# Kernel tuning notes

Measured on AMD Instinct MI355X. Metric: run time of the kernel, lower is better.

Reference implementation:

```python
import jax, jax.numpy as jnp
import numpy as np

B, L, D_MODEL, D_FF, N_EXPERTS, TOP_K = 32, 256, 512, 2048, 8, 2
EPS = 1e-9


def setup_inputs() -> dict:
    key = jax.random.key(0)
    ks = jax.random.split(key, 7)
    scale1 = 1.0 / np.sqrt(D_MODEL)
    scale2 = 1.0 / np.sqrt(D_FF)
    return {
        "cycle_curve_data": jax.random.normal(ks[0], (B, L, D_MODEL), jnp.float32),
        "logits": jax.random.normal(ks[1], (B, N_EXPERTS), jnp.float32),
        "moe_masks": jax.random.randint(ks[2], (B, N_EXPERTS), 0, 2, jnp.int32),
        "W1": jax.random.normal(ks[3], (N_EXPERTS, D_MODEL, D_FF), jnp.float32) * scale1,
        "b1": jax.random.normal(ks[4], (N_EXPERTS, D_FF), jnp.float32) * scale1,
        "W2": jax.random.normal(ks[5], (N_EXPERTS, D_FF, D_MODEL), jnp.float32) * scale2,
        "b2": jax.random.normal(ks[6], (N_EXPERTS, D_MODEL), jnp.float32) * scale2,
    }


def _gates(logits, moe_masks):
    # softmax over experts, zero out unavailable experts, keep top-k, renormalize
    mask = (moe_masks == 1).astype(logits.dtype)               # [B, E]
    p = jax.nn.softmax(logits, axis=1) * mask                  # [B, E]
    _, idx = jax.lax.top_k(p, TOP_K)                           # [B, K]
    topk_mask = jnp.zeros_like(p).at[jnp.arange(p.shape[0])[:, None], idx].set(1.0)
    p = p * topk_mask
    return p / (jnp.sum(p, axis=1, keepdims=True) + EPS)       # [B, E]


def reference(cycle_curve_data, logits, moe_masks, W1, b1, W2, b2):
    gates = _gates(logits, moe_masks)                          # [B, E]
    x = cycle_curve_data                                       # [B, L, D]
    # dense equivalent of per-expert gather -> MLP -> gate-weighted scatter-combine
    h = jnp.einsum("bld,edf->eblf", x, W1) + b1[:, None, None, :]   # [E,B,L,F]
    h = jax.nn.gelu(h, approximate=False)
    out = jnp.einsum("be,eblf,efd->bld", gates, h, W2)
    out = out + jnp.einsum("be,ed->bd", gates, b2)[:, None, :]      # [B,L,D]
    return out
```

## Files before the change

### kernel.cpp

```cpp
#include <hip/hip_runtime.h>

#define B_SZ 32
#define L_SZ 256
#define D_SZ 512
#define F_SZ 2048
#define E_SZ 8
#define P_SZ 64
#define BK2  32

typedef __attribute__((ext_vector_type(8)))  short bf16x8;
typedef __attribute__((ext_vector_type(16))) float f32x16;

__device__ __forceinline__ unsigned short f2bf(float f) {
  unsigned int u = __builtin_bit_cast(unsigned int, f);
  u += 0x7fffu + ((u >> 16) & 1u);
  return (unsigned short)(u >> 16);
}

__device__ __forceinline__ void async16(const void* g, void* l) {
  __builtin_amdgcn_global_load_lds(
      (const __attribute__((address_space(1))) unsigned int*)g,
      (__attribute__((address_space(3))) unsigned int*)l, 16, 0, 0);
}

__device__ __forceinline__ float gelu_f(float x) {
  float a = fabsf(x) * 0.70710678118654752f;
  float t = __builtin_amdgcn_rcpf(1.0f + 0.3275911f * a);
  float y = t * (0.254829592f +
            t * (-0.284496736f +
            t * (1.421413741f +
            t * (-1.453152027f +
            t * 1.061405429f))));
  float e = __expf(-a * a);
  float erf_abs = 1.0f - y * e;
  float erf_v = (x < 0.f) ? -erf_abs : erf_abs;
  return 0.5f * x * (1.0f + erf_v);
}

__device__ __forceinline__ void transpose_tile(
    const float* __restrict__ ip, unsigned short* __restrict__ op,
    int R, int C, int r0, int c0, float* tile, int tid) {
  int tx = tid & 63, ty = tid >> 6;
#pragma unroll
  for (int i = 0; i < 16; ++i) {
    int r = i * 4 + ty;
    tile[r * 65 + tx] = ip[(size_t)(r0 + r) * C + c0 + tx];
  }
  __syncthreads();
#pragma unroll
  for (int uu = 0; uu < 4; ++uu) {
    int u = uu * 256 + tid;
    int cc = u >> 4, q = u & 15;
    ushort4 o;
    o.x = f2bf(tile[(q * 4 + 0) * 65 + cc]);
    o.y = f2bf(tile[(q * 4 + 1) * 65 + cc]);
    o.z = f2bf(tile[(q * 4 + 2) * 65 + cc]);
    o.w = f2bf(tile[(q * 4 + 3) * 65 + cc]);
    *(ushort4*)(op + (size_t)(c0 + cc) * R + r0 + q * 4) = o;
  }
}

#define PREP_CONV_BLKS 4096
#define PREP_TR_BLKS   2048
#define PREP_TOTAL     (1 + PREP_CONV_BLKS + PREP_TR_BLKS)

__global__ __launch_bounds__(256) void prep_kernel(
    const float* __restrict__ logits, const int* __restrict__ masks,
    const float* __restrict__ x,
    const float* __restrict__ W1,
    int* __restrict__ sel_e, float* __restrict__ sel_g,
    unsigned short* __restrict__ xb,
    unsigned short* __restrict__ w1t) {
  __shared__ float tile[64 * 65];
  int blk = blockIdx.x;
  int tid = threadIdx.x;

  if (blk == 0) {
    int b = tid;
    if (b >= B_SZ) return;
    float lg[E_SZ], p[E_SZ];
    float mx = -1e30f;
    for (int e = 0; e < E_SZ; ++e) { lg[e] = logits[b * E_SZ + e]; mx = fmaxf(mx, lg[e]); }
    float s = 0.f;
    for (int e = 0; e < E_SZ; ++e) { p[e] = expf(lg[e] - mx); s += p[e]; }
    for (int e = 0; e < E_SZ; ++e) p[e] = (masks[b * E_SZ + e] == 1) ? (p[e] / s) : 0.f;
    int i0 = 0, i1 = 1; float v0 = -1.f, v1 = -1.f;
    for (int e = 0; e < E_SZ; ++e) {
      float v = p[e];
      if (v > v0)      { v1 = v0; i1 = i0; v0 = v; i0 = e; }
      else if (v > v1) { v1 = v;  i1 = e; }
    }
    float den = v0 + v1 + 1e-9f;
    sel_e[2 * b] = i0;  sel_e[2 * b + 1] = i1;
    sel_g[2 * b] = v0 / den;
    sel_g[2 * b + 1] = v1 / den;
    return;
  }
  blk -= 1;

  if (blk < PREP_CONV_BLKS) {
    int i = blk * 256 + tid;
    float4 v = ((const float4*)x)[i];
    ushort4 o;
    o.x = f2bf(v.x); o.y = f2bf(v.y); o.z = f2bf(v.z); o.w = f2bf(v.w);
    ((ushort4*)xb)[i] = o;
    return;
  }
  blk -= PREP_CONV_BLKS;

  int z = blk >> 8;
  int rem = blk & 255;
  int tr = rem >> 5, tc = rem & 31;
  transpose_tile(W1 + (size_t)z * D_SZ * F_SZ, w1t + (size_t)z * D_SZ * F_SZ,
                 D_SZ, F_SZ, tr * 64, tc * 64, tile, tid);
}

__global__ __launch_bounds__(256, 4) void moe_gemm1(
    const unsigned short* __restrict__ Xb,
    const unsigned short* __restrict__ W1t,
    const float* __restrict__ b1,
    const int* __restrict__ sel_e,
    unsigned short* __restrict__ H,
    const float* __restrict__ W2,
    unsigned short* __restrict__ w2t) {
  __shared__ __align__(16) char smem[32768];
  int tid = threadIdx.x;
  int lin = blockIdx.x;

  if (lin >= 2048) {
    int blk = lin - 2048;
    int z = blk >> 8;
    int rem = blk & 255;
    int tr = rem >> 3, tc = rem & 7;
    transpose_tile(W2 + (size_t)z * F_SZ * D_SZ, w2t + (size_t)z * F_SZ * D_SZ,
                   F_SZ, D_SZ, tr * 64, tc * 64, (float*)smem, tid);
    return;
  }

  unsigned short* As = (unsigned short*)smem;
  unsigned short* Bs = (unsigned short*)(smem + 16384);

  int f  = lin & 15;
  int l0 = ((lin >> 4) & 1) * 128;
  int p  = lin >> 5;
  int f0 = f * 128;
  int b  = p >> 1;
  int e  = sel_e[p];

  int lane = tid & 63;
  int w = tid >> 6, wm = w & 1, wn = w >> 1;
  int m32 = lane & 31, kh = lane >> 5;
  int sw = (m32 >> 1) & 3;

  const unsigned short* Abase = Xb  + ((size_t)b * L_SZ + l0) * D_SZ;
  const unsigned short* Bbase = W1t + ((size_t)e * F_SZ + f0) * D_SZ;

  int seg0 = w * 128 + lane;
  int row0 = seg0 >> 2, ks0 = ((seg0 & 3) ^ ((row0 >> 1) & 3)) * 8;
  int seg1 = seg0 + 64;
  int row1 = seg1 >> 2, ks1 = ((seg1 & 3) ^ ((row1 >> 1) & 3)) * 8;

  f32x16 acc[2][2] = {};

  for (int k0 = 0; k0 < D_SZ; k0 += 2 * BK2) {
#pragma unroll
    for (int h = 0; h < 2; ++h) {
      int kk = k0 + h * BK2;
      async16(Abase + (size_t)row0 * D_SZ + kk + ks0, &As[(h * 512 + seg0) * 8]);
      async16(Abase + (size_t)row1 * D_SZ + kk + ks1, &As[(h * 512 + seg1) * 8]);
      async16(Bbase + (size_t)row0 * D_SZ + kk + ks0, &Bs[(h * 512 + seg0) * 8]);
      async16(Bbase + (size_t)row1 * D_SZ + kk + ks1, &Bs[(h * 512 + seg1) * 8]);
    }
    __syncthreads();
#pragma unroll
    for (int h = 0; h < 2; ++h)
#pragma unroll
      for (int s = 0; s < 2; ++s) {
        int ko = ((((s << 1) | kh) ^ sw) << 3) + h * 4096;
        bf16x8 a0  = *(const bf16x8*)&As[(wm * 64 +      m32) * BK2 + ko];
        bf16x8 a1  = *(const bf16x8*)&As[(wm * 64 + 32 + m32) * BK2 + ko];
        bf16x8 b0  = *(const bf16x8*)&Bs[(wn * 64 +      m32) * BK2 + ko];
        bf16x8 b1f = *(const bf16x8*)&Bs[(wn * 64 + 32 + m32) * BK2 + ko];
        acc[0][0] = __builtin_amdgcn_mfma_f32_32x32x16_bf16(a0, b0,  acc[0][0], 0, 0, 0);
        acc[0][1] = __builtin_amdgcn_mfma_f32_32x32x16_bf16(a0, b1f, acc[0][1], 0, 0, 0);
        acc[1][0] = __builtin_amdgcn_mfma_f32_32x32x16_bf16(a1, b0,  acc[1][0], 0, 0, 0);
        acc[1][1] = __builtin_amdgcn_mfma_f32_32x32x16_bf16(a1, b1f, acc[1][1], 0, 0, 0);
      }
    __syncthreads();
  }

  float b1v[2];
#pragma unroll
  for (int tj = 0; tj < 2; ++tj)
    b1v[tj] = b1[e * F_SZ + f0 + wn * 64 + tj * 32 + m32];

  unsigned short* Hp = H + ((size_t)p * L_SZ + l0) * F_SZ + f0;
#pragma unroll
  for (int ti = 0; ti < 2; ++ti)
#pragma unroll
    for (int tj = 0; tj < 2; ++tj) {
      int col = wn * 64 + tj * 32 + m32;
#pragma unroll
      for (int r = 0; r < 16; ++r) {
        int row = wm * 64 + ti * 32 + (r & 3) + 8 * (r >> 2) + 4 * kh;
        Hp[(size_t)row * F_SZ + col] = f2bf(gelu_f(acc[ti][tj][r] + b1v[tj]));
      }
    }
}

__global__ __launch_bounds__(256, 4) void moe_gemm2(
    const unsigned short* __restrict__ H,
    const unsigned short* __restrict__ W2t,
    const float* __restrict__ b2,
    const int* __restrict__ sel_e,
    const float* __restrict__ sel_g,
    float* __restrict__ part,
    float* __restrict__ Out) {
  __shared__ __align__(16) unsigned short As[2][128 * BK2];
  __shared__ __align__(16) unsigned short Bs[2][128 * BK2];

  int lin = blockIdx.x;
  int q   = lin & 7;
  int d   = (lin >> 3) & 3;
  int g8  = lin >> 5;
  int gg  = g8 * 8 + q;
  int p   = gg >> 1;
  int l0  = (gg & 1) * 128;
  int d0  = d * 128;
  int b   = p >> 1;
  int e   = sel_e[p];
  float g = sel_g[p];

  int tid = threadIdx.x;
  int lane = tid & 63;
  int w = tid >> 6, wm = w & 1, wn = w >> 1;
  int m32 = lane & 31, kh = lane >> 5;
  int sw = (m32 >> 1) & 3;

  const unsigned short* Abase = H   + ((size_t)p * L_SZ + l0) * F_SZ;
  const unsigned short* Bbase = W2t + ((size_t)e * D_SZ + d0) * F_SZ;

  int seg0 = w * 128 + lane;
  int row0 = seg0 >> 2, ks0 = ((seg0 & 3) ^ ((row0 >> 1) & 3)) * 8;
  int seg1 = seg0 + 64;
  int row1 = seg1 >> 2, ks1 = ((seg1 & 3) ^ ((row1 >> 1) & 3)) * 8;

  f32x16 acc[2][2] = {};

  for (int k0 = 0; k0 < F_SZ; k0 += 2 * BK2) {
#pragma unroll
    for (int h = 0; h < 2; ++h) {
      int kk = k0 + h * BK2;
      async16(Abase + (size_t)row0 * F_SZ + kk + ks0, &As[h][seg0 * 8]);
      async16(Abase + (size_t)row1 * F_SZ + kk + ks1, &As[h][seg1 * 8]);
      async16(Bbase + (size_t)row0 * F_SZ + kk + ks0, &Bs[h][seg0 * 8]);
      async16(Bbase + (size_t)row1 * F_SZ + kk + ks1, &Bs[h][seg1 * 8]);
    }
    __syncthreads();
#pragma unroll
    for (int h = 0; h < 2; ++h)
#pragma unroll
      for (int s = 0; s < 2; ++s) {
        int ko = (((s << 1) | kh) ^ sw) << 3;
        bf16x8 a0  = *(const bf16x8*)&As[h][(wm * 64 +      m32) * BK2 + ko];
        bf16x8 a1  = *(const bf16x8*)&As[h][(wm * 64 + 32 + m32) * BK2 + ko];
        bf16x8 b0  = *(const bf16x8*)&Bs[h][(wn * 64 +      m32) * BK2 + ko];
        bf16x8 b1f = *(const bf16x8*)&Bs[h][(wn * 64 + 32 + m32) * BK2 + ko];
        acc[0][0] = __builtin_amdgcn_mfma_f32_32x32x16_bf16(a0, b0,  acc[0][0], 0, 0, 0);
        acc[0][1] = __builtin_amdgcn_mfma_f32_32x32x16_bf16(a0, b1f, acc[0][1], 0, 0, 0);
        acc[1][0] = __builtin_amdgcn_mfma_f32_32x32x16_bf16(a1, b0,  acc[1][0], 0, 0, 0);
        acc[1][1] = __builtin_amdgcn_mfma_f32_32x32x16_bf16(a1, b1f, acc[1][1], 0, 0, 0);
      }
    __syncthreads();
  }

  float bias[2] = {0.f, 0.f};
  if (p & 1) {
    int e0 = sel_e[2 * b], e1 = sel_e[2 * b + 1];
    float g0 = sel_g[2 * b], g1 = sel_g[2 * b + 1];
#pragma unroll
    for (int tj = 0; tj < 2; ++tj) {
      int dd = d0 + wn * 64 + tj * 32 + m32;
      bias[tj] = g0 * b2[e0 * D_SZ + dd] + g1 * b2[e1 * D_SZ + dd];
    }
  }
  float* dst = (p & 1) ? Out : part;
  float* Op = dst + ((size_t)b * L_SZ + l0) * D_SZ + d0;
#pragma unroll
  for (int ti = 0; ti < 2; ++ti)
#pragma unroll
    for (int tj = 0; tj < 2; ++tj) {
      int col = wn * 64 + tj * 32 + m32;
#pragma unroll
      for (int r = 0; r < 16; ++r) {
        int row = wm * 64 + ti * 32 + (r & 3) + 8 * (r >> 2) + 4 * kh;
        Op[(size_t)row * D_SZ + col] = g * acc[ti][tj][r] + bias[tj];
      }
    }
}

__global__ __launch_bounds__(256) void combine_kernel(
    const float* __restrict__ part, float* __restrict__ Out) {
  int i = blockIdx.x * 256 + threadIdx.x;
  float4 pv = ((const float4*)part)[i];
  float4 o  = ((float4*)Out)[i];
  o.x += pv.x; o.y += pv.y; o.z += pv.z; o.w += pv.w;
  ((float4*)Out)[i] = o;
}

extern "C" void kernel_launch(void* const* d_in, const int* in_sizes, int n_in,
                              void* d_out, int out_size, void* d_ws, size_t ws_size,
                              hipStream_t stream) {
  const float* x      = (const float*)d_in[0];
  const float* logits = (const float*)d_in[1];
  const int*   masks  = (const int*)d_in[2];
  const float* W1     = (const float*)d_in[3];
  const float* b1     = (const float*)d_in[4];
  const float* W2     = (const float*)d_in[5];
  const float* b2     = (const float*)d_in[6];
  float* out = (float*)d_out;

  char* ws = (char*)d_ws;
  int*   sel_e = (int*)ws;
  float* sel_g = (float*)(ws + 256);
  unsigned short* xb  = (unsigned short*)(ws + 1024);
  unsigned short* w1t = xb  + (size_t)B_SZ * L_SZ * D_SZ;
  unsigned short* w2t = w1t + (size_t)E_SZ * F_SZ * D_SZ;
  unsigned short* Hbuf = w2t + (size_t)E_SZ * D_SZ * F_SZ;
  float* part = (float*)(ws + 1024);

  prep_kernel<<<PREP_TOTAL, 256, 0, stream>>>(logits, masks, x, W1,
                                              sel_e, sel_g, xb, w1t);
  moe_gemm1<<<4096, 256, 0, stream>>>(xb, w1t, b1, sel_e, Hbuf, W2, w2t);
  moe_gemm2<<<512, 256, 0, stream>>>(Hbuf, w2t, b2, sel_e, sel_g, part, out);
  combine_kernel<<<(B_SZ * L_SZ * D_SZ / 4) / 256, 256, 0, stream>>>(part, out);
}
```

Measured before the change: 226.1 us.

## Enlarge MoE GEMM tiles to 128x256 and split-K GEMM2 with bf16 partials

Result: slower. 238.5 us (+5.5%).

```diff
diff --git a/kernel.cpp b/kernel.cpp
--- a/kernel.cpp
+++ b/kernel.cpp
@@ -15,6 +15,10 @@
   unsigned int u = __builtin_bit_cast(unsigned int, f);
   u += 0x7fffu + ((u >> 16) & 1u);
   return (unsigned short)(u >> 16);
+}
+__device__ __forceinline__ float bf2f(unsigned short s) {
+  unsigned int u = ((unsigned int)s) << 16;
+  return __builtin_bit_cast(float, u);
 }
 
 __device__ __forceinline__ void async16(const void* g, void* l) {
@@ -115,7 +119,7 @@
                  D_SZ, F_SZ, tr * 64, tc * 64, tile, tid);
 }
 
-__global__ __launch_bounds__(256, 4) void moe_gemm1(
+__global__ __launch_bounds__(256, 2) void moe_gemm1(
     const unsigned short* __restrict__ Xb,
     const unsigned short* __restrict__ W1t,
     const float* __restrict__ b1,
@@ -123,12 +127,12 @@
     unsigned short* __restrict__ H,
     const float* __restrict__ W2,
     unsigned short* __restrict__ w2t) {
-  __shared__ __align__(16) char smem[32768];
+  __shared__ __align__(16) char smem[49152];
   int tid = threadIdx.x;
   int lin = blockIdx.x;
 
-  if (lin >= 2048) {
-    int blk = lin - 2048;
+  if (lin >= 1024) {
+    int blk = lin - 1024;
     int z = blk >> 8;
     int rem = blk & 255;
     int tr = rem >> 3, tc = rem & 7;
@@ -140,10 +144,10 @@
   unsigned short* As = (unsigned short*)smem;
   unsigned short* Bs = (unsigned short*)(smem + 16384);
 
-  int f  = lin & 15;
-  int l0 = ((lin >> 4) & 1) * 128;
-  int p  = lin >> 5;
-  int f0 = f * 128;
+  int f  = lin & 7;
+  int l0 = ((lin >> 3) & 1) * 128;
+  int p  = lin >> 4;
+  int f0 = f * 256;
   int b  = p >> 1;
   int e  = sel_e[p];
 
@@ -155,81 +159,97 @@
   const unsigned short* Abase = Xb  + ((size_t)b * L_SZ + l0) * D_SZ;
   const unsigned short* Bbase = W1t + ((size_t)e * F_SZ + f0) * D_SZ;
 
-  int seg0 = w * 128 + lane;
-  int row0 = seg0 >> 2, ks0 = ((seg0 & 3) ^ ((row0 >> 1) & 3)) * 8;
-  int seg1 = seg0 + 64;
-  int row1 = seg1 >> 2, ks1 = ((seg1 & 3) ^ ((row1 >> 1) & 3)) * 8;
-
-  f32x16 acc[2][2] = {};
+  int arow[2], aks[2], brow[4], bks[4];
+#pragma unroll
+  for (int c = 0; c < 2; ++c) {
+    int seg = c * 256 + tid;
+    arow[c] = seg >> 2; aks[c] = ((seg & 3) ^ ((arow[c] >> 1) & 3)) * 8;
+  }
+#pragma unroll
+  for (int c = 0; c < 4; ++c) {
+    int seg = c * 256 + tid;
+    brow[c] = seg >> 2; bks[c] = ((seg & 3) ^ ((brow[c] >> 1) & 3)) * 8;
+  }
+
+  f32x16 acc[2][4] = {};
 
   for (int k0 = 0; k0 < D_SZ; k0 += 2 * BK2) {
 #pragma unroll
     for (int h = 0; h < 2; ++h) {
       int kk = k0 + h * BK2;
-      async16(Abase + (size_t)row0 * D_SZ + kk + ks0, &As[(h * 512 + seg0) * 8]);
-      async16(Abase + (size_t)row1 * D_SZ + kk + ks1, &As[(h * 512 + seg1) * 8]);
-      async16(Bbase + (size_t)row0 * D_SZ + kk + ks0, &Bs[(h * 512 + seg0) * 8]);
-      async16(Bbase + (size_t)row1 * D_SZ + kk + ks1, &Bs[(h * 512 + seg1) * 8]);
+#pragma unroll
+      for (int c = 0; c < 2; ++c)
+        async16(Abase + (size_t)arow[c] * D_SZ + kk + aks[c],
+                As + h * 4096 + (c * 256 + tid) * 8);
+#pragma unroll
+      for (int c = 0; c < 4; ++c)
+        async16(Bbase + (size_t)brow[c] * D_SZ + kk + bks[c],
+                Bs + h * 8192 + (c * 256 + tid) * 8);
     }
     __syncthreads();
 #pragma unroll
     for (int h = 0; h < 2; ++h)
 #pragma unroll
       for (int s = 0; s < 2; ++s) {
-        int ko = ((((s << 1) | kh) ^ sw) << 3) + h * 4096;
-        bf16x8 a0  = *(const bf16x8*)&As[(wm * 64 +      m32) * BK2 + ko];
-        bf16x8 a1  = *(const bf16x8*)&As[(wm * 64 + 32 + m32) * BK2 + ko];
-        bf16x8 b0  = *(const bf16x8*)&Bs[(wn * 64 +      m32) * BK2 + ko];
-        bf16x8 b1f = *(const bf16x8*)&Bs[(wn * 64 + 32 + m32) * BK2 + ko];
-        acc[0][0] = __builtin_amdgcn_mfma_f32_32x32x16_bf16(a0, b0,  acc[0][0], 0, 0, 0);
-        acc[0][1] = __builtin_amdgcn_mfma_f32_32x32x16_bf16(a0, b1f, acc[0][1], 0, 0, 0);
-        acc[1][0] = __builtin_amdgcn_mfma_f32_32x32x16_bf16(a1, b0,  acc[1][0], 0, 0, 0);
-        acc[1][1] = __builtin_amdgcn_mfma_f32_32x32x16_bf16(a1, b1f, acc[1][1], 0, 0, 0);
+        int ko = (((s << 1) | kh) ^ sw) << 3;
+        bf16x8 a[2], bb[4];
+#pragma unroll
+        for (int i = 0; i < 2; ++i)
+          a[i] = *(const bf16x8*)&As[h * 4096 + (wm * 64 + i * 32 + m32) * 32 + ko];
+#pragma unroll
+        for (int j = 0; j < 4; ++j)
+          bb[j] = *(const bf16x8*)&Bs[h * 8192 + (wn * 128 + j * 32 + m32) * 32 + ko];
+#pragma unroll
+        for (int i = 0; i < 2; ++i)
+#pragma unroll
+          for (int j = 0; j < 4; ++j)
+            acc[i][j] = __builtin_amdgcn_mfma_f32_32x32x16_bf16(a[i], bb[j], acc[i][j], 0, 0, 0);
       }
     __syncthreads();
   }
 
-  float b1v[2];
-#pragma unroll
-  for (int tj = 0; tj < 2; ++tj)
-    b1v[tj] = b1[e * F_SZ + f0 + wn * 64 + tj * 32 + m32];
+  float b1v[4];
+#pragma unroll
+  for (int j = 0; j < 4; ++j)
+    b1v[j] = b1[e * F_SZ + f0 + wn * 128 + j * 32 + m32];
 
   unsigned short* Hp = H + ((size_t)p * L_SZ + l0) * F_SZ + f0;
 #pragma unroll
-  for (int ti = 0; ti < 2; ++ti)
-#pragma unroll
-    for (int tj = 0; tj < 2; ++tj) {
-      int col = wn * 64 + tj * 32 + m32;
+  for (int i = 0; i < 2; ++i)
+#pragma unroll
+    for (int j = 0; j < 4; ++j) {
+      int col = wn * 128 + j * 32 + m32;
 #pragma unroll
       for (int r = 0; r < 16; ++r) {
-        int row = wm * 64 + ti * 32 + (r & 3) + 8 * (r >> 2) + 4 * kh;
-        Hp[(size_t)row * F_SZ + col] = f2bf(gelu_f(acc[ti][tj][r] + b1v[tj]));
+        int row = wm * 64 + i * 32 + (r & 3) + 8 * (r >> 2) + 4 * kh;
+        Hp[(size_t)row * F_SZ + col] = f2bf(gelu_f(acc[i][j][r] + b1v[j]));
       }
     }
 }
 
-__global__ __launch_bounds__(256, 4) void moe_gemm2(
+__global__ __launch_bounds__(256, 2) void moe_gemm2(
     const unsigned short* __restrict__ H,
     const unsigned short* __restrict__ W2t,
-    const float* __restrict__ b2,
     const int* __restrict__ sel_e,
     const float* __restrict__ sel_g,
-    float* __restrict__ part,
+    unsigned short* __restrict__ part0,
+    unsigned short* __restrict__ part1,
+    unsigned short* __restrict__ part2,
     float* __restrict__ Out) {
-  __shared__ __align__(16) unsigned short As[2][128 * BK2];
-  __shared__ __align__(16) unsigned short Bs[2][128 * BK2];
+  __shared__ __align__(16) char smem[49152];
+  unsigned short* As = (unsigned short*)smem;
+  unsigned short* Bs = (unsigned short*)(smem + 16384);
 
   int lin = blockIdx.x;
-  int q   = lin & 7;
-  int d   = (lin >> 3) & 3;
-  int g8  = lin >> 5;
-  int gg  = g8 * 8 + q;
-  int p   = gg >> 1;
-  int l0  = (gg & 1) * 128;
-  int d0  = d * 128;
+  int d   = lin & 1;
+  int kq  = (lin >> 1) & 1;
+  int l0  = ((lin >> 2) & 1) * 128;
+  int p   = lin >> 3;
+  int d0  = d * 256;
   int b   = p >> 1;
   int e   = sel_e[p];
   float g = sel_g[p];
+  int kbase = kq * (F_SZ / 2);
 
   int tid = threadIdx.x;
   int lane = tid & 63;
@@ -237,24 +257,35 @@
   int m32 = lane & 31, kh = lane >> 5;
   int sw = (m32 >> 1) & 3;
 
-  const unsigned short* Abase = H   + ((size_t)p * L_SZ + l0) * F_SZ;
-  const unsigned short* Bbase = W2t + ((size_t)e * D_SZ + d0) * F_SZ;
-
-  int seg0 = w * 128 + lane;
-  int row0 = seg0 >> 2, ks0 = ((seg0 & 3) ^ ((row0 >> 1) & 3)) * 8;
-  int seg1 = seg0 + 64;
-  int row1 = seg1 >> 2, ks1 = ((seg1 & 3) ^ ((row1 >> 1) & 3)) * 8;
-
-  f32x16 acc[2][2] = {};
-
-  for (int k0 = 0; k0 < F_SZ; k0 += 2 * BK2) {
+  const unsigned short* Abase = H   + ((size_t)p * L_SZ + l0) * F_SZ + kbase;
+  const unsigned short* Bbase = W2t + ((size_t)e * D_SZ + d0) * F_SZ + kbase;
+
+  int arow[2], aks[2], brow[4], bks[4];
+#pragma unroll
+  for (int c = 0; c < 2; ++c) {
+    int seg = c * 256 + tid;
+    arow[c] = seg >> 2; aks[c] = ((seg & 3) ^ ((arow[c] >> 1) & 3)) * 8;
+  }
+#pragma unroll
+  for (int c = 0; c < 4; ++c) {
+    int seg = c * 256 + tid;
+    brow[c] = seg >> 2; bks[c] = ((seg & 3) ^ ((brow[c] >> 1) & 3)) * 8;
+  }
+
+  f32x16 acc[2][4] = {};
+
+  for (int k0 = 0; k0 < F_SZ / 2; k0 += 2 * BK2) {
 #pragma unroll
     for (int h = 0; h < 2; ++h) {
       int kk = k0 + h * BK2;
-      async16(Abase + (size_t)row0 * F_SZ + kk + ks0, &As[h][seg0 * 8]);
-      async16(Abase + (size_t)row1 * F_SZ + kk + ks1, &As[h][seg1 * 8]);
-      async16(Bbase + (size_t)row0 * F_SZ + kk + ks0, &Bs[h][seg0 * 8]);
-      async16(Bbase + (size_t)row1 * F_SZ + kk + ks1, &Bs[h][seg1 * 8]);
+#pragma unroll
+      for (int c = 0; c < 2; ++c)
+        async16(Abase + (size_t)arow[c] * F_SZ + kk + aks[c],
+                As + h * 4096 + (c * 256 + tid) * 8);
+#pragma unroll
+      for (int c = 0; c < 4; ++c)
+        async16(Bbase + (size_t)brow[c] * F_SZ + kk + bks[c],
+                Bs + h * 8192 + (c * 256 + tid) * 8);
     }
     __syncthreads();
 #pragma unroll
@@ -262,49 +293,75 @@
 #pragma unroll
       for (int s = 0; s < 2; ++s) {
         int ko = (((s << 1) | kh) ^ sw) << 3;
-        bf16x8 a0  = *(const bf16x8*)&As[h][(wm * 64 +      m32) * BK2 + ko];
-        bf16x8 a1  = *(const bf16x8*)&As[h][(wm * 64 + 32 + m32) * BK2 + ko];
-        bf16x8 b0  = *(const bf16x8*)&Bs[h][(wn * 64 +      m32) * BK2 + ko];
-        bf16x8 b1f = *(const bf16x8*)&Bs[h][(wn * 64 + 32 + m32) * BK2 + ko];
-        acc[0][0] = __builtin_amdgcn_mfma_f32_32x32x16_bf16(a0, b0,  acc[0][0], 0, 0, 0);
-        acc[0][1] = __builtin_amdgcn_mfma_f32_32x32x16_bf16(a0, b1f, acc[0][1], 0, 0, 0);
-        acc[1][0] = __builtin_amdgcn_mfma_f32_32x32x16_bf16(a1, b0,  acc[1][0], 0, 0, 0);
-        acc[1][1] = __builtin_amdgcn_mfma_f32_32x32x16_bf16(a1, b1f, acc[1][1], 0, 0, 0);
+        bf16x8 a[2], bb[4];
+#pragma unroll
+        for (int i = 0; i < 2; ++i)
+          a[i] = *(const bf16x8*)&As[h * 4096 + (wm * 64 + i * 32 + m32) * 32 + ko];
+#pragma unroll
+        for (int j = 0; j < 4; ++j)
+          bb[j] = *(const bf16x8*)&Bs[h * 8192 + (wn * 128 + j * 32 + m32) * 32 + ko];
+#pragma unroll
+        for (int i = 0; i < 2; ++i)
+#pragma unroll
+          for (int j = 0; j < 4; ++j)
+            acc[i][j] = __builtin_amdgcn_mfma_f32_32x32x16_bf16(a[i], bb[j], acc[i][j], 0, 0, 0);
       }
     __syncthreads();
   }
 
-  float bias[2] = {0.f, 0.f};
-  if (p & 1) {
-    int e0 = sel_e[2 * b], e1 = sel_e[2 * b + 1];
-    float g0 = sel_g[2 * b], g1 = sel_g[2 * b + 1];
-#pragma unroll
-    for (int tj = 0; tj < 2; ++tj) {
-      int dd = d0 + wn * 64 + tj * 32 + m32;
-      bias[tj] = g0 * b2[e0 * D_SZ + dd] + g1 * b2[e1 * D_SZ + dd];
-    }
-  }
-  float* dst = (p & 1) ? Out : part;
-  float* Op = dst + ((size_t)b * L_SZ + l0) * D_SZ + d0;
-#pragma unroll
-  for (int ti = 0; ti < 2; ++ti)
-#pragma unroll
-    for (int tj = 0; tj < 2; ++tj) {
-      int col = wn * 64 + tj * 32 + m32;
-#pragma unroll
-      for (int r = 0; r < 16; ++r) {
-        int row = wm * 64 + ti * 32 + (r & 3) + 8 * (r >> 2) + 4 * kh;
-        Op[(size_t)row * D_SZ + col] = g * acc[ti][tj][r] + bias[tj];
-      }
-    }
+  int role = (p & 1) * 2 + kq;
+  size_t obase = ((size_t)b * L_SZ + l0) * D_SZ + d0;
+  if (role == 3) {
+    float* Op = Out + obase;
+#pragma unroll
+    for (int i = 0; i < 2; ++i)
+#pragma unroll
+      for (int j = 0; j < 4; ++j) {
+        int col = wn * 128 + j * 32 + m32;
+#pragma unroll
+        for (int r = 0; r < 16; ++r) {
+          int row = wm * 64 + i * 32 + (r & 3) + 8 * (r >> 2) + 4 * kh;
+          Op[(size_t)row * D_SZ + col] = g * acc[i][j][r];
+        }
+      }
+  } else {
+    unsigned short* Pp = (role == 0 ? part0 : (role == 1 ? part1 : part2)) + obase;
+#pragma unroll
+    for (int i = 0; i < 2; ++i)
+#pragma unroll
+      for (int j = 0; j < 4; ++j) {
+        int col = wn * 128 + j * 32 + m32;
+#pragma unroll
+        for (int r = 0; r < 16; ++r) {
+          int row = wm * 64 + i * 32 + (r & 3) + 8 * (r >> 2) + 4 * kh;
+          Pp[(size_t)row * D_SZ + col] = f2bf(g * acc[i][j][r]);
+        }
+      }
+  }
 }
 
 __global__ __launch_bounds__(256) void combine_kernel(
-    const float* __restrict__ part, float* __restrict__ Out) {
+    const unsigned short* __restrict__ part0,
+    const unsigned short* __restrict__ part1,
+    const unsigned short* __restrict__ part2,
+    const float* __restrict__ b2,
+    const int* __restrict__ sel_e, const float* __restrict__ sel_g,
+    float* __restrict__ Out) {
   int i = blockIdx.x * 256 + threadIdx.x;
-  float4 pv = ((const float4*)part)[i];
-  float4 o  = ((float4*)Out)[i];
-  o.x += pv.x; o.y += pv.y; o.z += pv.z; o.w += pv.w;
+  int d4 = i & (D_SZ / 4 - 1);
+  int b  = i >> 15;
+  int e0 = sel_e[2 * b], e1 = sel_e[2 * b + 1];
+  float g0 = sel_g[2 * b], g1 = sel_g[2 * b + 1];
+  ushort4 p0 = ((const ushort4*)part0)[i];
+  ushort4 p1 = ((const ushort4*)part1)[i];
+  ushort4 p2 = ((const ushort4*)part2)[i];
+  float4 o   = ((float4*)Out)[i];
+  float4 v0 = ((const float4*)(b2 + (size_t)e0 * D_SZ))[d4];
+  float4 v1 = ((const float4*)(b2 + (size_t)e1 * D_SZ))[d4];
+  o.x += bf2f(p0.x) + bf2f(p1.x) + bf2f(p2.x) + g0 * v0.x + g1 * v1.x;
+  o.y += bf2f(p0.y) + bf2f(p1.y) + bf2f(p2.y) + g0 * v0.y + g1 * v1.y;
+  o.z += bf2f(p0.z) + bf2f(p1.z) + bf2f(p2.z) + g0 * v0.z + g1 * v1.z;
+  o.w += bf2f(p0.w) + bf2f(p1.w) + bf2f(p2.w) + g0 * v0.w + g1 * v1.w;
   ((float4*)Out)[i] = o;
 }
 
@@ -327,11 +384,15 @@
   unsigned short* w1t = xb  + (size_t)B_SZ * L_SZ * D_SZ;
   unsigned short* w2t = w1t + (size_t)E_SZ * F_SZ * D_SZ;
   unsigned short* Hbuf = w2t + (size_t)E_SZ * D_SZ * F_SZ;
-  float* part = (float*)(ws + 1024);
+  unsigned short* part0 = (unsigned short*)(ws + 1024);
+  unsigned short* part1 = part0 + (size_t)B_SZ * L_SZ * D_SZ;
+  unsigned short* part2 = part1 + (size_t)B_SZ * L_SZ * D_SZ;
 
   prep_kernel<<<PREP_TOTAL, 256, 0, stream>>>(logits, masks, x, W1,
                                               sel_e, sel_g, xb, w1t);
-  moe_gemm1<<<4096, 256, 0, stream>>>(xb, w1t, b1, sel_e, Hbuf, W2, w2t);
-  moe_gemm2<<<512, 256, 0, stream>>>(Hbuf, w2t, b2, sel_e, sel_g, part, out);
-  combine_kernel<<<(B_SZ * L_SZ * D_SZ / 4) / 256, 256, 0, stream>>>(part, out);
-}
+  moe_gemm1<<<3072, 256, 0, stream>>>(xb, w1t, b1, sel_e, Hbuf, W2, w2t);
+  moe_gemm2<<<512, 256, 0, stream>>>(Hbuf, w2t, sel_e, sel_g,
+                                     part0, part1, part2, out);
+  combine_kernel<<<(B_SZ * L_SZ * D_SZ / 4) / 256, 256, 0, stream>>>(
+      part0, part1, part2, b2, sel_e, sel_g, out);
+}
```

## Split-K the second MoE GEMM in two and store partials in bf16

Applied to the files above, without the earlier changes.

New measurement: 231.9 us. 2.6% more time.

```diff
diff --git a/kernel.cpp b/kernel.cpp
--- a/kernel.cpp
+++ b/kernel.cpp
@@ -15,6 +15,10 @@
   unsigned int u = __builtin_bit_cast(unsigned int, f);
   u += 0x7fffu + ((u >> 16) & 1u);
   return (unsigned short)(u >> 16);
+}
+__device__ __forceinline__ float bf2f(unsigned short s) {
+  unsigned int u = ((unsigned int)s) << 16;
+  return __builtin_bit_cast(float, u);
 }
 
 __device__ __forceinline__ void async16(const void* g, void* l) {
@@ -211,18 +215,21 @@
 __global__ __launch_bounds__(256, 4) void moe_gemm2(
     const unsigned short* __restrict__ H,
     const unsigned short* __restrict__ W2t,
-    const float* __restrict__ b2,
     const int* __restrict__ sel_e,
     const float* __restrict__ sel_g,
-    float* __restrict__ part,
+    unsigned short* __restrict__ part0,
+    unsigned short* __restrict__ part1,
+    unsigned short* __restrict__ part2,
     float* __restrict__ Out) {
   __shared__ __align__(16) unsigned short As[2][128 * BK2];
   __shared__ __align__(16) unsigned short Bs[2][128 * BK2];
 
   int lin = blockIdx.x;
-  int q   = lin & 7;
-  int d   = (lin >> 3) & 3;
-  int g8  = lin >> 5;
+  int kq  = lin >> 9;
+  int l9  = lin & 511;
+  int q   = l9 & 7;
+  int d   = (l9 >> 3) & 3;
+  int g8  = l9 >> 5;
   int gg  = g8 * 8 + q;
   int p   = gg >> 1;
   int l0  = (gg & 1) * 128;
@@ -230,6 +237,7 @@
   int b   = p >> 1;
   int e   = sel_e[p];
   float g = sel_g[p];
+  int kbase = kq * (F_SZ / 2);
 
   int tid = threadIdx.x;
   int lane = tid & 63;
@@ -237,8 +245,8 @@
   int m32 = lane & 31, kh = lane >> 5;
   int sw = (m32 >> 1) & 3;
 
-  const unsigned short* Abase = H   + ((size_t)p * L_SZ + l0) * F_SZ;
-  const unsigned short* Bbase = W2t + ((size_t)e * D_SZ + d0) * F_SZ;
+  const unsigned short* Abase = H   + ((size_t)p * L_SZ + l0) * F_SZ + kbase;
+  const unsigned short* Bbase = W2t + ((size_t)e * D_SZ + d0) * F_SZ + kbase;
 
   int seg0 = w * 128 + lane;
   int row0 = seg0 >> 2, ks0 = ((seg0 & 3) ^ ((row0 >> 1) & 3)) * 8;
@@ -247,7 +255,7 @@
 
   f32x16 acc[2][2] = {};
 
-  for (int k0 = 0; k0 < F_SZ; k0 += 2 * BK2) {
+  for (int k0 = 0; k0 < F_SZ / 2; k0 += 2 * BK2) {
 #pragma unroll
     for (int h = 0; h < 2; ++h) {
       int kk = k0 + h * BK2;
@@ -274,37 +282,60 @@
     __syncthreads();
   }
 
-  float bias[2] = {0.f, 0.f};
-  if (p & 1) {
-    int e0 = sel_e[2 * b], e1 = sel_e[2 * b + 1];
-    float g0 = sel_g[2 * b], g1 = sel_g[2 * b + 1];
-#pragma unroll
-    for (int tj = 0; tj < 2; ++tj) {
-      int dd = d0 + wn * 64 + tj * 32 + m32;
-      bias[tj] = g0 * b2[e0 * D_SZ + dd] + g1 * b2[e1 * D_SZ + dd];
-    }
-  }
-  float* dst = (p & 1) ? Out : part;
-  float* Op = dst + ((size_t)b * L_SZ + l0) * D_SZ + d0;
-#pragma unroll
-  for (int ti = 0; ti < 2; ++ti)
-#pragma unroll
-    for (int tj = 0; tj < 2; ++tj) {
-      int col = wn * 64 + tj * 32 + m32;
-#pragma unroll
-      for (int r = 0; r < 16; ++r) {
-        int row = wm * 64 + ti * 32 + (r & 3) + 8 * (r >> 2) + 4 * kh;
-        Op[(size_t)row * D_SZ + col] = g * acc[ti][tj][r] + bias[tj];
-      }
-    }
+  int role = (p & 1) * 2 + kq;
+  size_t obase = ((size_t)b * L_SZ + l0) * D_SZ + d0;
+  if (role == 3) {
+    float* Op = Out + obase;
+#pragma unroll
+    for (int ti = 0; ti < 2; ++ti)
+#pragma unroll
+      for (int tj = 0; tj < 2; ++tj) {
+        int col = wn * 64 + tj * 32 + m32;
+#pragma unroll
+        for (int r = 0; r < 16; ++r) {
+          int row = wm * 64 + ti * 32 + (r & 3) + 8 * (r >> 2) + 4 * kh;
+          Op[(size_t)row * D_SZ + col] = g * acc[ti][tj][r];
+        }
+      }
+  } else {
+    unsigned short* Pp =
+        (role == 0 ? part0 : (role == 1 ? part1 : part2)) + obase;
+#pragma unroll
+    for (int ti = 0; ti < 2; ++ti)
+#pragma unroll
+      for (int tj = 0; tj < 2; ++tj) {
+        int col = wn * 64 + tj * 32 + m32;
+#pragma unroll
+        for (int r = 0; r < 16; ++r) {
+          int row = wm * 64 + ti * 32 + (r & 3) + 8 * (r >> 2) + 4 * kh;
+          Pp[(size_t)row * D_SZ + col] = f2bf(g * acc[ti][tj][r]);
+        }
+      }
+  }
 }
 
 __global__ __launch_bounds__(256) void combine_kernel(
-    const float* __restrict__ part, float* __restrict__ Out) {
+    const unsigned short* __restrict__ part0,
+    const unsigned short* __restrict__ part1,
+    const unsigned short* __restrict__ part2,
+    const float* __restrict__ b2,
+    const int* __restrict__ sel_e, const float* __restrict__ sel_g,
+    float* __restrict__ Out) {
   int i = blockIdx.x * 256 + threadIdx.x;
-  float4 pv = ((const float4*)part)[i];
-  float4 o  = ((float4*)Out)[i];
-  o.x += pv.x; o.y += pv.y; o.z += pv.z; o.w += pv.w;
+  int d4 = i & (D_SZ / 4 - 1);
+  int b  = i >> 15;
+  int e0 = sel_e[2 * b], e1 = sel_e[2 * b + 1];
+  float g0 = sel_g[2 * b], g1 = sel_g[2 * b + 1];
+  ushort4 p0 = ((const ushort4*)part0)[i];
+  ushort4 p1 = ((const ushort4*)part1)[i];
+  ushort4 p2 = ((const ushort4*)part2)[i];
+  float4 o   = ((float4*)Out)[i];
+  float4 v0 = ((const float4*)(b2 + (size_t)e0 * D_SZ))[d4];
+  float4 v1 = ((const float4*)(b2 + (size_t)e1 * D_SZ))[d4];
+  o.x += bf2f(p0.x) + bf2f(p1.x) + bf2f(p2.x) + g0 * v0.x + g1 * v1.x;
+  o.y += bf2f(p0.y) + bf2f(p1.y) + bf2f(p2.y) + g0 * v0.y + g1 * v1.y;
+  o.z += bf2f(p0.z) + bf2f(p1.z) + bf2f(p2.z) + g0 * v0.z + g1 * v1.z;
+  o.w += bf2f(p0.w) + bf2f(p1.w) + bf2f(p2.w) + g0 * v0.w + g1 * v1.w;
   ((float4*)Out)[i] = o;
 }
 
@@ -327,11 +358,15 @@
   unsigned short* w1t = xb  + (size_t)B_SZ * L_SZ * D_SZ;
   unsigned short* w2t = w1t + (size_t)E_SZ * F_SZ * D_SZ;
   unsigned short* Hbuf = w2t + (size_t)E_SZ * D_SZ * F_SZ;
-  float* part = (float*)(ws + 1024);
+  unsigned short* part0 = (unsigned short*)(ws + 1024);
+  unsigned short* part1 = part0 + (size_t)B_SZ * L_SZ * D_SZ;
+  unsigned short* part2 = part1 + (size_t)B_SZ * L_SZ * D_SZ;
 
   prep_kernel<<<PREP_TOTAL, 256, 0, stream>>>(logits, masks, x, W1,
                                               sel_e, sel_g, xb, w1t);
   moe_gemm1<<<4096, 256, 0, stream>>>(xb, w1t, b1, sel_e, Hbuf, W2, w2t);
-  moe_gemm2<<<512, 256, 0, stream>>>(Hbuf, w2t, b2, sel_e, sel_g, part, out);
-  combine_kernel<<<(B_SZ * L_SZ * D_SZ / 4) / 256, 256, 0, stream>>>(part, out);
-}
+  moe_gemm2<<<1024, 256, 0, stream>>>(Hbuf, w2t, sel_e, sel_g,
+                                      part0, part1, part2, out);
+  combine_kernel<<<(B_SZ * L_SZ * D_SZ / 4) / 256, 256, 0, stream>>>(
+      part0, part1, part2, b2, sel_e, sel_g, out);
+}
```
